# Performance work log

Measured on AMD Instinct MI355X. Metric: run time of the kernel, lower is better.

The kernel has to match this reference:

```python
import jax, jax.numpy as jnp
import numpy as np

B, S, ENC, DEC = 32, 4096, 512, 512


def setup_inputs() -> dict:
    key = jax.random.key(0)
    k1, k2, k3, k4, k5 = jax.random.split(key, 5)
    return {
        "decoder_hidden": jax.random.normal(k1, (B, DEC), dtype=jnp.float32),
        "encoder_outputs": jax.random.normal(k2, (B, S, ENC), dtype=jnp.float32),
        "W_attn": jax.random.normal(k3, (DEC, ENC + DEC), dtype=jnp.float32) * (1.0 / np.sqrt(ENC + DEC)),
        "b_attn": jax.random.normal(k4, (DEC,), dtype=jnp.float32) * 0.01,
        "v": jax.random.normal(k5, (DEC,), dtype=jnp.float32) * (1.0 / np.sqrt(DEC)),
    }


def reference(decoder_hidden, encoder_outputs, W_attn, b_attn, v):
    dec_dim = decoder_hidden.shape[-1]
    # torch concatenates (hidden, encoder_outputs) then applies attn;
    # algebraically equivalent split avoids materializing the repeat+concat.
    W_h = W_attn[:, :dec_dim]   # [dec, dec]
    W_e = W_attn[:, dec_dim:]   # [dec, enc]
    # [B, 1, dec] + [B, S, dec] + [dec]
    proj = (jnp.einsum('bd,ed->be', decoder_hidden, W_h)[:, None, :]
            + jnp.einsum('bse,de->bsd', encoder_outputs, W_e)
            + b_attn)
    energy = jnp.tanh(proj)                      # [B, S, dec]
    scores = jnp.einsum('bsd,d->bs', energy, v)  # [B, S]
    return jax.nn.softmax(scores, axis=1)
```

## Files before the change

### kernel.cpp

```cpp
#include <hip/hip_runtime.h>
#include <hip/hip_bf16.h>
#include <stdint.h>


typedef __attribute__((ext_vector_type(8))) short short8;
typedef __attribute__((ext_vector_type(4))) float f32x4;

static __device__ __forceinline__ unsigned short f2bf(float f) {
    union { float f; uint32_t u; } x{f};
    uint32_t u = x.u;
    u += 0x7fffu + ((u >> 16) & 1u);
    return (unsigned short)(u >> 16);
}

static __device__ __forceinline__ float tanh_fast(float x) {
    return 1.0f - 2.0f / (__expf(2.0f * x) + 1.0f);
}

__global__ __launch_bounds__(512) void prep_kernel(
    const float* __restrict__ dh, const float* __restrict__ W_attn,
    const float* __restrict__ b_attn, unsigned short* __restrict__ wsB,
    float* __restrict__ wsP1) {
    __shared__ float dhs[512];
    const int tid = threadIdx.x;
    if (blockIdx.x < 64) {
        int idx = blockIdx.x * 512 + tid;
        int c8 = idx & 7;
        int n  = (idx >> 3) & 511;
        int kt = idx >> 12;
        const float* src = W_attn + (size_t)n * 1024 + 512 + kt * 64 + c8 * 8;
        float4 f0 = *(const float4*)(src);
        float4 f1 = *(const float4*)(src + 4);
        short8 p;
        p[0] = (short)f2bf(f0.x); p[1] = (short)f2bf(f0.y);
        p[2] = (short)f2bf(f0.z); p[3] = (short)f2bf(f0.w);
        p[4] = (short)f2bf(f1.x); p[5] = (short)f2bf(f1.y);
        p[6] = (short)f2bf(f1.z); p[7] = (short)f2bf(f1.w);
        int row = kt * 512 + n;
        int byteInRow = (c8 * 16) ^ ((n & 7) << 4);
        *(short8*)((char*)wsB + (size_t)row * 128 + byteInRow) = p;
    } else {
        int b = blockIdx.x - 64;
        dhs[tid] = dh[b * 512 + tid];
        __syncthreads();
        const float* wrow = W_attn + (size_t)tid * 1024;
        float acc = 0.f;
        #pragma unroll 8
        for (int d = 0; d < 512; d += 4) {
            float4 w = *(const float4*)(wrow + d);
            acc += dhs[d] * w.x + dhs[d + 1] * w.y + dhs[d + 2] * w.z + dhs[d + 3] * w.w;
        }
        wsP1[b * 512 + tid] = acc + b_attn[tid];
    }
}

__global__ __launch_bounds__(256, 3) void fused_kernel(
    const float* __restrict__ enc, const unsigned short* __restrict__ wsB,
    const float* __restrict__ wsP1, const float* __restrict__ vvec,
    float* __restrict__ out, float* __restrict__ wsS1) {
    __shared__ char lds[40960];
    char* const A_lds = lds;
    char* const B_lds = lds + 8192;

    const int tid  = threadIdx.x;
    const int wc   = tid >> 6;
    const int lane = tid & 63;
    const int llo  = lane & 15, lhi = lane >> 4;

    const int bid = blockIdx.x;
    const int lb  = (bid & 7) * 512 + (bid >> 3);
    const int rb  = lb >> 1, cb = lb & 1;
    const int m0  = rb * 64;
    const int b   = m0 >> 12;

    const int ar = tid >> 2, ac = tid & 3;
    const float* aptr = enc + (size_t)(m0 + ar) * 512 + ac * 16;
    const int aoff0 = ar * 128 + (((ac * 32)     ) ^ ((ar & 7) << 4));
    const int aoff1 = ar * 128 + (((ac * 32) + 16) ^ ((ar & 7) << 4));
    const char* bbase = (const char*)wsB + cb * 32768;

    f32x4 acc[4][4] = {};
    float4 fa0, fa1, fa2, fa3;

    #define A_LOAD(kt)                                 \
        do { const float* p_ = aptr + (kt) * 64;       \
             fa0 = *(const float4*)(p_);               \
             fa1 = *(const float4*)(p_ + 4);           \
             fa2 = *(const float4*)(p_ + 8);           \
             fa3 = *(const float4*)(p_ + 12); } while (0)

    #define A_WRITE()                                                    \
        do { short8 p0_, p1_;                                            \
             p0_[0]=(short)f2bf(fa0.x); p0_[1]=(short)f2bf(fa0.y);       \
             p0_[2]=(short)f2bf(fa0.z); p0_[3]=(short)f2bf(fa0.w);       \
             p0_[4]=(short)f2bf(fa1.x); p0_[5]=(short)f2bf(fa1.y);       \
             p0_[6]=(short)f2bf(fa1.z); p0_[7]=(short)f2bf(fa1.w);       \
             p1_[0]=(short)f2bf(fa2.x); p1_[1]=(short)f2bf(fa2.y);       \
             p1_[2]=(short)f2bf(fa2.z); p1_[3]=(short)f2bf(fa2.w);       \
             p1_[4]=(short)f2bf(fa3.x); p1_[5]=(short)f2bf(fa3.y);       \
             p1_[6]=(short)f2bf(fa3.z); p1_[7]=(short)f2bf(fa3.w);       \
             *(short8*)(A_lds + aoff0) = p0_;                            \
             *(short8*)(A_lds + aoff1) = p1_; } while (0)

    #define B_GLDS(kt)                                                             \
        do { const char* bsrc_ = bbase + (size_t)(kt) * 65536;                     \
             _Pragma("unroll")                                                     \
             for (int i_ = 0; i_ < 8; ++i_) {                                      \
                 int off_ = i_ * 4096 + wc * 1024;                                 \
                 __builtin_amdgcn_global_load_lds(                                 \
                     (const uint32_t __attribute__((address_space(1)))*)(bsrc_ + off_ + lane * 16), \
                     (uint32_t __attribute__((address_space(3)))*)(B_lds + off_),  \
                     16, 0, 0);                                                    \
             } } while (0)

    #define COMPUTE()                                                              \
        do { _Pragma("unroll")                                                     \
             for (int kk = 0; kk < 2; ++kk) {                                      \
                 const int gbyte = kk * 64 + lhi * 16;                             \
                 short8 af[4], bfr[4];                                             \
                 _Pragma("unroll")                                                 \
                 for (int mi = 0; mi < 4; ++mi) {                                  \
                     int row = mi * 16 + llo;                                      \
                     af[mi] = *(const short8*)(A_lds + row * 128 +                 \
                                               (gbyte ^ ((row & 7) << 4)));        \
                 }                                                                 \
                 _Pragma("unroll")                                                 \
                 for (int ni = 0; ni < 4; ++ni) {                                  \
                     int n = wc * 64 + ni * 16 + llo;                              \
                     bfr[ni] = *(const short8*)(B_lds + n * 128 +                  \
                                                (gbyte ^ ((n & 7) << 4)));         \
                 }                                                                 \
                 _Pragma("unroll")                                                 \
                 for (int mi = 0; mi < 4; ++mi)                                    \
                     _Pragma("unroll")                                             \
                     for (int ni = 0; ni < 4; ++ni)                                \
                         acc[mi][ni] = __builtin_amdgcn_mfma_f32_16x16x32_bf16(    \
                             af[mi], bfr[ni], acc[mi][ni], 0, 0, 0);               \
             } } while (0)

    A_LOAD(0);
    A_WRITE();
    B_GLDS(0);
    __syncthreads();

    #pragma unroll
    for (int kt = 0; kt < 8; ++kt) {
        if (kt < 7) A_LOAD(kt + 1);
        COMPUTE();
        __syncthreads();
        if (kt < 7) {
            A_WRITE();
            B_GLDS(kt + 1);
            __syncthreads();
        }
    }

    float p1v[4], vv[4];
    #pragma unroll
    for (int ni = 0; ni < 4; ++ni) {
        int d = cb * 256 + wc * 64 + ni * 16 + llo;
        p1v[ni] = wsP1[b * 512 + d];
        vv[ni]  = vvec[d];
    }
    float part[16];
    #pragma unroll
    for (int mi = 0; mi < 4; ++mi)
        #pragma unroll
        for (int r = 0; r < 4; ++r) {
            float s = 0.f;
            #pragma unroll
            for (int ni = 0; ni < 4; ++ni)
                s += tanh_fast(acc[mi][ni][r] + p1v[ni]) * vv[ni];
            part[mi * 4 + r] = s;
        }
    #pragma unroll
    for (int off = 1; off < 16; off <<= 1)
        #pragma unroll
        for (int i = 0; i < 16; ++i)
            part[i] += __shfl_xor(part[i], off, 64);

    float* red = (float*)lds;
    if (llo == 0) {
        #pragma unroll
        for (int mi = 0; mi < 4; ++mi)
            #pragma unroll
            for (int r = 0; r < 4; ++r)
                red[wc * 64 + mi * 16 + lhi * 4 + r] = part[mi * 4 + r];
    }
    __syncthreads();
    if (tid < 64) {
        float s = red[tid] + red[64 + tid] + red[128 + tid] + red[192 + tid];
        (cb ? wsS1 : out)[m0 + tid] = s;
    }
}

__global__ __launch_bounds__(256) void softmax_kernel(
    float* __restrict__ out, const float* __restrict__ wsS1) {
    __shared__ float wred[8];
    const int b = blockIdx.x, tid = threadIdx.x;
    float* row = out + (size_t)b * 4096;
    const float* row1 = wsS1 + (size_t)b * 4096;
    float vals[16];
    float lmax = -1e30f;
    #pragma unroll
    for (int i = 0; i < 16; ++i) {
        vals[i] = row[i * 256 + tid] + row1[i * 256 + tid];
        lmax = fmaxf(lmax, vals[i]);
    }
    #pragma unroll
    for (int off = 32; off >= 1; off >>= 1)
        lmax = fmaxf(lmax, __shfl_xor(lmax, off, 64));
    if ((tid & 63) == 0) wred[tid >> 6] = lmax;
    __syncthreads();
    float gmax = fmaxf(fmaxf(wred[0], wred[1]), fmaxf(wred[2], wred[3]));
    float lsum = 0.f;
    #pragma unroll
    for (int i = 0; i < 16; ++i) {
        vals[i] = expf(vals[i] - gmax);
        lsum += vals[i];
    }
    #pragma unroll
    for (int off = 32; off >= 1; off >>= 1)
        lsum += __shfl_xor(lsum, off, 64);
    if ((tid & 63) == 0) wred[4 + (tid >> 6)] = lsum;
    __syncthreads();
    float inv = 1.f / (wred[4] + wred[5] + wred[6] + wred[7]);
    #pragma unroll
    for (int i = 0; i < 16; ++i)
        row[i * 256 + tid] = vals[i] * inv;
}

extern "C" void kernel_launch(void* const* d_in, const int* in_sizes, int n_in,
                              void* d_out, int out_size, void* d_ws, size_t ws_size,
                              hipStream_t stream) {
    const float* dh   = (const float*)d_in[0];
    const float* enc  = (const float*)d_in[1];
    const float* Wat  = (const float*)d_in[2];
    const float* batt = (const float*)d_in[3];
    const float* vvec = (const float*)d_in[4];
    float* out = (float*)d_out;

    unsigned short* wsB = (unsigned short*)d_ws;
    float* wsP1 = (float*)((char*)d_ws + 524288);
    float* wsS1 = (float*)((char*)d_ws + 589824);

    hipLaunchKernelGGL(prep_kernel, dim3(96), dim3(512), 0, stream,
                       dh, Wat, batt, wsB, wsP1);
    hipLaunchKernelGGL(fused_kernel, dim3(4096), dim3(256), 0, stream,
                       enc, wsB, wsP1, vvec, out, wsS1);
    hipLaunchKernelGGL(softmax_kernel, dim3(32), dim3(256), 0, stream, out, wsS1);
}
```

Before: 145.3 us.

## Read B fragments directly from global, double-buffer A tile in LDS

The B (weight) operand no longer goes through LDS. Each lane loads its MFMA fragments straight from a plain row-major bf16 weight buffer, which removes the global-to-LDS copies and shrinks LDS from 40 KB to 16 KB. The A tile is now double-buffered, so only one barrier per k-step is needed instead of two, and the bf16 conversion uses the packed __float22bfloat162_rn intrinsic. The trade-off is that B fragments are re-read from global/L2 by each block with less coalesced 16-byte accesses, while the smaller LDS footprint may allow higher occupancy.

```diff
diff --git a/kernel.cpp b/kernel.cpp
--- a/kernel.cpp
+++ b/kernel.cpp
@@ -6,11 +6,13 @@
 typedef __attribute__((ext_vector_type(8))) short short8;
 typedef __attribute__((ext_vector_type(4))) float f32x4;
 
-static __device__ __forceinline__ unsigned short f2bf(float f) {
-    union { float f; uint32_t u; } x{f};
-    uint32_t u = x.u;
-    u += 0x7fffu + ((u >> 16) & 1u);
-    return (unsigned short)(u >> 16);
+static __device__ __forceinline__ short8 cvt8(float4 a, float4 b) {
+    union { short8 s; __hip_bfloat162 h[4]; } u;
+    u.h[0] = __float22bfloat162_rn(float2{a.x, a.y});
+    u.h[1] = __float22bfloat162_rn(float2{a.z, a.w});
+    u.h[2] = __float22bfloat162_rn(float2{b.x, b.y});
+    u.h[3] = __float22bfloat162_rn(float2{b.z, b.w});
+    return u.s;
 }
 
 static __device__ __forceinline__ float tanh_fast(float x) {
@@ -25,20 +27,12 @@
     const int tid = threadIdx.x;
     if (blockIdx.x < 64) {
         int idx = blockIdx.x * 512 + tid;
-        int c8 = idx & 7;
-        int n  = (idx >> 3) & 511;
-        int kt = idx >> 12;
-        const float* src = W_attn + (size_t)n * 1024 + 512 + kt * 64 + c8 * 8;
+        int n  = idx >> 6;
+        int c8 = idx & 63;
+        const float* src = W_attn + (size_t)n * 1024 + 512 + c8 * 8;
         float4 f0 = *(const float4*)(src);
         float4 f1 = *(const float4*)(src + 4);
-        short8 p;
-        p[0] = (short)f2bf(f0.x); p[1] = (short)f2bf(f0.y);
-        p[2] = (short)f2bf(f0.z); p[3] = (short)f2bf(f0.w);
-        p[4] = (short)f2bf(f1.x); p[5] = (short)f2bf(f1.y);
-        p[6] = (short)f2bf(f1.z); p[7] = (short)f2bf(f1.w);
-        int row = kt * 512 + n;
-        int byteInRow = (c8 * 16) ^ ((n & 7) << 4);
-        *(short8*)((char*)wsB + (size_t)row * 128 + byteInRow) = p;
+        *(short8*)((char*)wsB + (size_t)n * 1024 + c8 * 16) = cvt8(f0, f1);
     } else {
         int b = blockIdx.x - 64;
         dhs[tid] = dh[b * 512 + tid];
@@ -58,9 +52,8 @@
     const float* __restrict__ enc, const unsigned short* __restrict__ wsB,
     const float* __restrict__ wsP1, const float* __restrict__ vvec,
     float* __restrict__ out, float* __restrict__ wsS1) {
-    __shared__ char lds[40960];
-    char* const A_lds = lds;
-    char* const B_lds = lds + 8192;
+    __shared__ char lds[16384];
+    char* const Ab[2] = { lds, lds + 8192 };
 
     const int tid  = threadIdx.x;
     const int wc   = tid >> 6;
@@ -77,7 +70,9 @@
     const float* aptr = enc + (size_t)(m0 + ar) * 512 + ac * 16;
     const int aoff0 = ar * 128 + (((ac * 32)     ) ^ ((ar & 7) << 4));
     const int aoff1 = ar * 128 + (((ac * 32) + 16) ^ ((ar & 7) << 4));
-    const char* bbase = (const char*)wsB + cb * 32768;
+
+    const char* blane = (const char*)wsB +
+                        (size_t)(cb * 256 + wc * 64 + llo) * 1024 + lhi * 16;
 
     f32x4 acc[4][4] = {};
     float4 fa0, fa1, fa2, fa3;
@@ -89,70 +84,46 @@
              fa2 = *(const float4*)(p_ + 8);           \
              fa3 = *(const float4*)(p_ + 12); } while (0)
 
-    #define A_WRITE()                                                    \
-        do { short8 p0_, p1_;                                            \
-             p0_[0]=(short)f2bf(fa0.x); p0_[1]=(short)f2bf(fa0.y);       \
-             p0_[2]=(short)f2bf(fa0.z); p0_[3]=(short)f2bf(fa0.w);       \
-             p0_[4]=(short)f2bf(fa1.x); p0_[5]=(short)f2bf(fa1.y);       \
-             p0_[6]=(short)f2bf(fa1.z); p0_[7]=(short)f2bf(fa1.w);       \
-             p1_[0]=(short)f2bf(fa2.x); p1_[1]=(short)f2bf(fa2.y);       \
-             p1_[2]=(short)f2bf(fa2.z); p1_[3]=(short)f2bf(fa2.w);       \
-             p1_[4]=(short)f2bf(fa3.x); p1_[5]=(short)f2bf(fa3.y);       \
-             p1_[6]=(short)f2bf(fa3.z); p1_[7]=(short)f2bf(fa3.w);       \
-             *(short8*)(A_lds + aoff0) = p0_;                            \
-             *(short8*)(A_lds + aoff1) = p1_; } while (0)
-
-    #define B_GLDS(kt)                                                             \
-        do { const char* bsrc_ = bbase + (size_t)(kt) * 65536;                     \
+    #define A_WRITE(Adst)                              \
+        do { *(short8*)((Adst) + aoff0) = cvt8(fa0, fa1); \
+             *(short8*)((Adst) + aoff1) = cvt8(fa2, fa3); } while (0)
+
+    #define COMPUTE(Asrc, kt)                                                      \
+        do { const char* bk_ = blane + (kt) * 128;                                 \
+             short8 bfr[8];                                                        \
              _Pragma("unroll")                                                     \
-             for (int i_ = 0; i_ < 8; ++i_) {                                      \
-                 int off_ = i_ * 4096 + wc * 1024;                                 \
-                 __builtin_amdgcn_global_load_lds(                                 \
-                     (const uint32_t __attribute__((address_space(1)))*)(bsrc_ + off_ + lane * 16), \
-                     (uint32_t __attribute__((address_space(3)))*)(B_lds + off_),  \
-                     16, 0, 0);                                                    \
-             } } while (0)
-
-    #define COMPUTE()                                                              \
-        do { _Pragma("unroll")                                                     \
+             for (int ni = 0; ni < 4; ++ni) {                                      \
+                 bfr[ni * 2]     = *(const short8*)(bk_ + ni * 16384);             \
+                 bfr[ni * 2 + 1] = *(const short8*)(bk_ + ni * 16384 + 64);        \
+             }                                                                     \
+             _Pragma("unroll")                                                     \
              for (int kk = 0; kk < 2; ++kk) {                                      \
                  const int gbyte = kk * 64 + lhi * 16;                             \
-                 short8 af[4], bfr[4];                                             \
+                 short8 af[4];                                                     \
                  _Pragma("unroll")                                                 \
                  for (int mi = 0; mi < 4; ++mi) {                                  \
                      int row = mi * 16 + llo;                                      \
-                     af[mi] = *(const short8*)(A_lds + row * 128 +                 \
+                     af[mi] = *(const short8*)((Asrc) + row * 128 +                \
                                                (gbyte ^ ((row & 7) << 4)));        \
-                 }                                                                 \
-                 _Pragma("unroll")                                                 \
-                 for (int ni = 0; ni < 4; ++ni) {                                  \
-                     int n = wc * 64 + ni * 16 + llo;                              \
-                     bfr[ni] = *(const short8*)(B_lds + n * 128 +                  \
-                                                (gbyte ^ ((n & 7) << 4)));         \
                  }                                                                 \
                  _Pragma("unroll")                                                 \
                  for (int mi = 0; mi < 4; ++mi)                                    \
                      _Pragma("unroll")                                             \
                      for (int ni = 0; ni < 4; ++ni)                                \
                          acc[mi][ni] = __builtin_amdgcn_mfma_f32_16x16x32_bf16(    \
-                             af[mi], bfr[ni], acc[mi][ni], 0, 0, 0);               \
+                             af[mi], bfr[ni * 2 + kk], acc[mi][ni], 0, 0, 0);      \
              } } while (0)
 
     A_LOAD(0);
-    A_WRITE();
-    B_GLDS(0);
+    A_WRITE(Ab[0]);
     __syncthreads();
 
     #pragma unroll
     for (int kt = 0; kt < 8; ++kt) {
         if (kt < 7) A_LOAD(kt + 1);
-        COMPUTE();
+        COMPUTE(Ab[kt & 1], kt);
+        if (kt < 7) A_WRITE(Ab[(kt + 1) & 1]);
         __syncthreads();
-        if (kt < 7) {
-            A_WRITE();
-            B_GLDS(kt + 1);
-            __syncthreads();
-        }
     }
 
     float p1v[4], vv[4];
```

New measurement: 220.8 us. +52.0%, slower.

## Double-buffer A tile in LDS with manual waitcnt pipelining and hardware bf16 conversion

Applied to the files above, without the earlier changes.

Adds a second LDS buffer for the bf16 A tile so the next tile can be written while the current one is read, and prefetches A two iterations ahead. Replaces __syncthreads with explicit s_waitcnt plus s_barrier fenced by sched_barrier, so outstanding global loads can overlap compute. Also swaps the manual bit-twiddling float-to-bf16 rounding for the packed __float22bfloat162_rn intrinsic. The cost is more LDS per block (48 KB), which may limit occupancy, and the hand-written vmcnt counts must exactly match the number of in-flight loads.

```diff
diff --git a/kernel.cpp b/kernel.cpp
--- a/kernel.cpp
+++ b/kernel.cpp
@@ -6,11 +6,13 @@
 typedef __attribute__((ext_vector_type(8))) short short8;
 typedef __attribute__((ext_vector_type(4))) float f32x4;
 
-static __device__ __forceinline__ unsigned short f2bf(float f) {
-    union { float f; uint32_t u; } x{f};
-    uint32_t u = x.u;
-    u += 0x7fffu + ((u >> 16) & 1u);
-    return (unsigned short)(u >> 16);
+static __device__ __forceinline__ short8 cvt8(float4 a, float4 b) {
+    union { short8 s; __hip_bfloat162 h[4]; } u;
+    u.h[0] = __float22bfloat162_rn(float2{a.x, a.y});
+    u.h[1] = __float22bfloat162_rn(float2{a.z, a.w});
+    u.h[2] = __float22bfloat162_rn(float2{b.x, b.y});
+    u.h[3] = __float22bfloat162_rn(float2{b.z, b.w});
+    return u.s;
 }
 
 static __device__ __forceinline__ float tanh_fast(float x) {
@@ -31,14 +33,9 @@
         const float* src = W_attn + (size_t)n * 1024 + 512 + kt * 64 + c8 * 8;
         float4 f0 = *(const float4*)(src);
         float4 f1 = *(const float4*)(src + 4);
-        short8 p;
-        p[0] = (short)f2bf(f0.x); p[1] = (short)f2bf(f0.y);
-        p[2] = (short)f2bf(f0.z); p[3] = (short)f2bf(f0.w);
-        p[4] = (short)f2bf(f1.x); p[5] = (short)f2bf(f1.y);
-        p[6] = (short)f2bf(f1.z); p[7] = (short)f2bf(f1.w);
         int row = kt * 512 + n;
         int byteInRow = (c8 * 16) ^ ((n & 7) << 4);
-        *(short8*)((char*)wsB + (size_t)row * 128 + byteInRow) = p;
+        *(short8*)((char*)wsB + (size_t)row * 128 + byteInRow) = cvt8(f0, f1);
     } else {
         int b = blockIdx.x - 64;
         dhs[tid] = dh[b * 512 + tid];
@@ -58,9 +55,8 @@
     const float* __restrict__ enc, const unsigned short* __restrict__ wsB,
     const float* __restrict__ wsP1, const float* __restrict__ vvec,
     float* __restrict__ out, float* __restrict__ wsS1) {
-    __shared__ char lds[40960];
-    char* const A_lds = lds;
-    char* const B_lds = lds + 8192;
+    __shared__ char lds[49152];
+    char* const B_lds = lds + 16384;
 
     const int tid  = threadIdx.x;
     const int wc   = tid >> 6;
@@ -81,6 +77,9 @@
 
     f32x4 acc[4][4] = {};
     float4 fa0, fa1, fa2, fa3;
+
+    #define SCHEDB() __builtin_amdgcn_sched_barrier(0)
+    #define BAR() __builtin_amdgcn_s_barrier()
 
     #define A_LOAD(kt)                                 \
         do { const float* p_ = aptr + (kt) * 64;       \
@@ -89,18 +88,9 @@
              fa2 = *(const float4*)(p_ + 8);           \
              fa3 = *(const float4*)(p_ + 12); } while (0)
 
-    #define A_WRITE()                                                    \
-        do { short8 p0_, p1_;                                            \
-             p0_[0]=(short)f2bf(fa0.x); p0_[1]=(short)f2bf(fa0.y);       \
-             p0_[2]=(short)f2bf(fa0.z); p0_[3]=(short)f2bf(fa0.w);       \
-             p0_[4]=(short)f2bf(fa1.x); p0_[5]=(short)f2bf(fa1.y);       \
-             p0_[6]=(short)f2bf(fa1.z); p0_[7]=(short)f2bf(fa1.w);       \
-             p1_[0]=(short)f2bf(fa2.x); p1_[1]=(short)f2bf(fa2.y);       \
-             p1_[2]=(short)f2bf(fa2.z); p1_[3]=(short)f2bf(fa2.w);       \
-             p1_[4]=(short)f2bf(fa3.x); p1_[5]=(short)f2bf(fa3.y);       \
-             p1_[6]=(short)f2bf(fa3.z); p1_[7]=(short)f2bf(fa3.w);       \
-             *(short8*)(A_lds + aoff0) = p0_;                            \
-             *(short8*)(A_lds + aoff1) = p1_; } while (0)
+    #define A_WRITE(Adst)                              \
+        do { *(short8*)((Adst) + aoff0) = cvt8(fa0, fa1); \
+             *(short8*)((Adst) + aoff1) = cvt8(fa2, fa3); } while (0)
 
     #define B_GLDS(kt)                                                             \
         do { const char* bsrc_ = bbase + (size_t)(kt) * 65536;                     \
@@ -113,7 +103,7 @@
                      16, 0, 0);                                                    \
              } } while (0)
 
-    #define COMPUTE()                                                              \
+    #define COMPUTE(Asrc)                                                          \
         do { _Pragma("unroll")                                                     \
              for (int kk = 0; kk < 2; ++kk) {                                      \
                  const int gbyte = kk * 64 + lhi * 16;                             \
@@ -121,7 +111,7 @@
                  _Pragma("unroll")                                                 \
                  for (int mi = 0; mi < 4; ++mi) {                                  \
                      int row = mi * 16 + llo;                                      \
-                     af[mi] = *(const short8*)(A_lds + row * 128 +                 \
+                     af[mi] = *(const short8*)((Asrc) + row * 128 +                \
                                                (gbyte ^ ((row & 7) << 4)));        \
                  }                                                                 \
                  _Pragma("unroll")                                                 \
@@ -139,21 +129,29 @@
              } } while (0)
 
     A_LOAD(0);
-    A_WRITE();
+    A_WRITE(lds);
     B_GLDS(0);
-    __syncthreads();
-
-    #pragma unroll
-    for (int kt = 0; kt < 8; ++kt) {
-        if (kt < 7) A_LOAD(kt + 1);
-        COMPUTE();
-        __syncthreads();
-        if (kt < 7) {
-            A_WRITE();
-            B_GLDS(kt + 1);
-            __syncthreads();
+    A_LOAD(1);
+    asm volatile("s_waitcnt vmcnt(4) lgkmcnt(0)" ::: "memory");
+    SCHEDB(); BAR(); SCHEDB();
+
+    #pragma unroll 1
+    for (int kt = 0; kt < 7; ++kt) {
+        COMPUTE(lds + (kt & 1) * 8192);
+        A_WRITE(lds + ((kt + 1) & 1) * 8192);
+        asm volatile("s_waitcnt lgkmcnt(0)" ::: "memory");
+        SCHEDB(); BAR(); SCHEDB();
+        B_GLDS(kt + 1);
+        if (kt < 6) {
+            A_LOAD(kt + 2);
+            asm volatile("s_waitcnt vmcnt(4)" ::: "memory");
+        } else {
+            asm volatile("s_waitcnt vmcnt(0)" ::: "memory");
         }
-    }
+        SCHEDB(); BAR(); SCHEDB();
+    }
+    COMPUTE(lds + 8192);
+    __syncthreads();
 
     float p1v[4], vv[4];
     #pragma unroll
```

After: 146.9 us. About the same (+1.1%).
